# Optimization experiments

Hardware: AMD Instinct MI355X
Metric: run time of the kernel (lower is better)

The kernel has to match this reference:

```python
import jax, jax.numpy as jnp
import numpy as np

NUM_HEADS = 32
NUM_KV = 8
HEAD_DIM = 128


def rotate_half(x):
    half = x.shape[-1] // 2
    x1, x2 = x[..., :half], x[..., half:]
    return jnp.concatenate([-x2, x1], axis=-1)


def apply_rope(x, cos, sin):
    # x: [B, H, S, D]; cos/sin: [S, D] broadcast over batch and heads
    return x * cos + rotate_half(x) * sin


def setup_inputs() -> dict:
    key = jax.random.key(0)
    kx, kqkv, kout = jax.random.split(key, 3)
    B, S, H = 2, 2048, 4096
    x = jax.random.normal(kx, (B, S, H), dtype=jnp.float32)
    Wqkv = jax.random.normal(kqkv, (H, NUM_HEADS * HEAD_DIM + 2 * NUM_KV * HEAD_DIM), dtype=jnp.float32) * (H ** -0.5)
    Wout = jax.random.normal(kout, (H, H), dtype=jnp.float32) * (H ** -0.5)
    # realistic RoPE tables (seq, head_dim)
    inv_freq = 1.0 / (10000.0 ** (np.arange(0, HEAD_DIM, 2, dtype=np.float32) / HEAD_DIM))
    freqs = np.outer(np.arange(S, dtype=np.float32), inv_freq)  # [S, D/2]
    emb = np.concatenate([freqs, freqs], axis=-1)  # [S, D]
    cos = jnp.asarray(np.cos(emb), dtype=jnp.float32)
    sin = jnp.asarray(np.sin(emb), dtype=jnp.float32)
    return {"x": x, "cos": cos, "sin": sin, "Wqkv": Wqkv, "Wout": Wout}


def reference(x, cos, sin, Wqkv, Wout):
    B, S, H = x.shape
    nh, nkv, hd = NUM_HEADS, NUM_KV, HEAD_DIM
    qkv = x @ Wqkv  # [B, S, (nh+2*nkv)*hd]
    q, k, v = jnp.split(qkv, [nh * hd, nh * hd + nkv * hd], axis=-1)
    q = q.reshape(B, S, nh, hd).transpose(0, 2, 1, 3)   # [B, nh, S, hd]
    k = k.reshape(B, S, nkv, hd).transpose(0, 2, 1, 3)  # [B, nkv, S, hd]
    v = v.reshape(B, S, nkv, hd).transpose(0, 2, 1, 3)
    q = apply_rope(q, cos, sin)
    k = apply_rope(k, cos, sin)
    group = nh // nkv
    k = jnp.repeat(k, group, axis=1)  # repeat_interleave over head dim
    v = jnp.repeat(v, group, axis=1)
    scale = 1.0 / jnp.sqrt(jnp.asarray(hd, dtype=x.dtype))
    scores = jnp.einsum('bhqd,bhkd->bhqk', q, k) * scale  # [B, nh, S, S]
    causal = jnp.triu(jnp.ones((S, S), dtype=bool), k=1)
    scores = jnp.where(causal, -jnp.inf, scores)
    w = jax.nn.softmax(scores, axis=-1)
    out = jnp.einsum('bhqk,bhkd->bhqd', w, v)  # [B, nh, S, hd]
    out = out.transpose(0, 2, 1, 3).reshape(B, S, nh * hd)
    return out @ Wout
```

## Files before the change

kernel.cpp:

```cpp
#include <hip/hip_runtime.h>

typedef unsigned short u16;
typedef __attribute__((ext_vector_type(8))) short s16x8;
typedef __attribute__((ext_vector_type(4))) short s16x4;
typedef __attribute__((ext_vector_type(4))) float f32x4;

#define DEVI __device__ __forceinline__

DEVI u16 f2b(float f) {
  union { float f; unsigned u; } v; v.f = f;
  unsigned r = v.u + 0x7FFFu + ((v.u >> 16) & 1u);
  return (u16)(r >> 16);
}
DEVI float b2f(u16 h) {
  union { unsigned u; float f; } v; v.u = ((unsigned)h) << 16;
  return v.f;
}

typedef const __attribute__((address_space(1))) void gas_void;
typedef __attribute__((address_space(3))) void las_void;
DEVI void gload16(const void* g, void* l) {
  __builtin_amdgcn_global_load_lds((gas_void*)g, (las_void*)l, 16, 0, 0);
}

__global__ void conv_bf16(const float* __restrict__ in, u16* __restrict__ out, int n8) {
  int i = blockIdx.x * 256 + threadIdx.x;
  if (i >= n8) return;
  const float* p = in + (size_t)i * 8;
  float4 u = *(const float4*)p;
  float4 v = *(const float4*)(p + 4);
  s16x8 o = {(short)f2b(u.x), (short)f2b(u.y), (short)f2b(u.z), (short)f2b(u.w),
             (short)f2b(v.x), (short)f2b(v.y), (short)f2b(v.z), (short)f2b(v.w)};
  *(s16x8*)(out + (size_t)i * 8) = o;
}

__global__ void trans_bf16(const float* __restrict__ W, u16* __restrict__ Wt, int K, int N) {
  __shared__ __attribute__((aligned(16))) u16 tile[64][68];
  const int t = threadIdx.x;
  const int n0 = blockIdx.x * 64, k0 = blockIdx.y * 64;
#pragma unroll
  for (int i = 0; i < 4; ++i) {
    int c = i * 256 + t;
    int r = c >> 4, q = c & 15;
    float4 v = *(const float4*)(W + (size_t)(k0 + r) * N + n0 + q * 4);
    s16x4 o = {(short)f2b(v.x), (short)f2b(v.y), (short)f2b(v.z), (short)f2b(v.w)};
    *(s16x4*)&tile[r][q * 4] = o;
  }
  __syncthreads();
#pragma unroll
  for (int i = 0; i < 2; ++i) {
    int c = i * 256 + t;
    int n_ = c >> 3, ck = (c & 7) * 8;
    s16x8 o;
#pragma unroll
    for (int j = 0; j < 8; ++j) o[j] = (short)tile[ck + j][n_];
    *(s16x8*)(Wt + (size_t)(n0 + n_) * K + k0 + ck) = o;
  }
}

template <typename TC>
__global__ __launch_bounds__(512, 2) void gemm256(const u16* __restrict__ A,
                                                  const u16* __restrict__ Bt,
                                                  TC* __restrict__ C, int M, int N, int K) {
  __shared__ __attribute__((aligned(16))) u16 As[2][256 * 64];
  __shared__ __attribute__((aligned(16))) u16 Bs[2][256 * 64];
  const int t = threadIdx.x;
  const int nbn = N >> 8;
  const int nwg = (M >> 8) * nbn;
  const int chunk = nwg >> 3;
  const int id = (blockIdx.x & 7) * chunk + (blockIdx.x >> 3);
  const int row0 = (id / nbn) << 8, col0 = (id % nbn) << 8;
  const int w = t >> 6, lane = t & 63, lc = lane & 15, lg = lane >> 4;
  const int wm = (w >> 2) * 128, wn = (w & 3) * 64;
  const int sw7 = lc & 7;

  const f32x4 FZ = {0.f, 0.f, 0.f, 0.f};
  f32x4 acc[8][4];
#pragma unroll
  for (int i = 0; i < 8; ++i)
#pragma unroll
    for (int j = 0; j < 4; ++j) acc[i][j] = FZ;

  const int c_r[4] = {t >> 3, (512 + t) >> 3, (1024 + t) >> 3, (1536 + t) >> 3};
  const int c_s = t & 7;

#define ISSUE_A(i, kt, slot)                                                            \
  gload16(A + (size_t)(row0 + c_r[i]) * K + ((kt) << 6) + ((c_s ^ (c_r[i] & 7)) << 3),  \
          (u16*)As[slot] + ((i) * 512 + t) * 8)
#define ISSUE_B(i, kt, slot)                                                            \
  gload16(Bt + (size_t)(col0 + c_r[i]) * K + ((kt) << 6) + ((c_s ^ (c_r[i] & 7)) << 3), \
          (u16*)Bs[slot] + ((i) * 512 + t) * 8)
#define LOAD_A(MH, AC)                                                            \
  _Pragma("unroll") for (int mf = 0; mf < 4; ++mf)                                \
  _Pragma("unroll") for (int ks = 0; ks < 2; ++ks)                                \
    af[mf][ks] = *(const s16x8*)((AC) + (wm + (MH)*64 + mf * 16 + lc) * 64 +      \
                                 (((ks * 4 + lg) ^ sw7) << 3));
#define LOAD_B(NH, BC)                                                            \
  _Pragma("unroll") for (int nf = 0; nf < 2; ++nf)                                \
  _Pragma("unroll") for (int ks = 0; ks < 2; ++ks)                                \
    bfv[nf][ks] = *(const s16x8*)((BC) + (wn + (NH)*32 + nf * 16 + lc) * 64 +     \
                                  (((ks * 4 + lg) ^ sw7) << 3));
#define MFMA_Q(MH, NH)                                                            \
  _Pragma("unroll") for (int ks = 0; ks < 2; ++ks)                                \
  _Pragma("unroll") for (int mf = 0; mf < 4; ++mf)                                \
  _Pragma("unroll") for (int nf = 0; nf < 2; ++nf)                                \
    acc[(MH)*4 + mf][(NH)*2 + nf] = __builtin_amdgcn_mfma_f32_16x16x32_bf16(      \
        af[mf][ks], bfv[nf][ks], acc[(MH)*4 + mf][(NH)*2 + nf], 0, 0, 0);
#define BAR __builtin_amdgcn_s_barrier()
#define PRIO1 __builtin_amdgcn_s_setprio(1)
#define PRIO0 __builtin_amdgcn_s_setprio(0)

  s16x8 af[4][2], bfv[2][2];
  const int NT = K >> 6;

  ISSUE_A(0, 0, 0); ISSUE_A(1, 0, 0); ISSUE_A(2, 0, 0); ISSUE_A(3, 0, 0);
  ISSUE_B(0, 0, 0); ISSUE_B(1, 0, 0); ISSUE_B(2, 0, 0); ISSUE_B(3, 0, 0);
  asm volatile("s_waitcnt vmcnt(0)" ::: "memory");
  BAR;

  for (int kt = 0; kt < NT; ++kt) {
    const int cur = kt & 1, nxt = cur ^ 1;
    const u16* Ac = As[cur];
    const u16* Bc = Bs[cur];
    LOAD_A(0, Ac)
    LOAD_B(0, Bc)
    if (kt + 1 < NT) {
      ISSUE_A(0, kt + 1, nxt); ISSUE_A(1, kt + 1, nxt);
      ISSUE_A(2, kt + 1, nxt); ISSUE_A(3, kt + 1, nxt);
      ISSUE_B(0, kt + 1, nxt); ISSUE_B(1, kt + 1, nxt);
      ISSUE_B(2, kt + 1, nxt); ISSUE_B(3, kt + 1, nxt);
    }
    BAR; PRIO1; MFMA_Q(0, 0); PRIO0; BAR;
    LOAD_B(1, Bc)
    BAR; PRIO1; MFMA_Q(0, 1); PRIO0; BAR;
    LOAD_A(1, Ac)
    BAR; PRIO1; MFMA_Q(1, 1); PRIO0; BAR;
    LOAD_B(0, Bc)
    BAR; PRIO1; MFMA_Q(1, 0); PRIO0;
    asm volatile("s_waitcnt vmcnt(0)" ::: "memory");
    BAR;
  }
#undef ISSUE_A
#undef ISSUE_B
#undef LOAD_A
#undef LOAD_B
#undef MFMA_Q
#undef BAR
#undef PRIO1
#undef PRIO0

#pragma unroll
  for (int am = 0; am < 8; ++am)
#pragma unroll
    for (int an = 0; an < 4; ++an)
#pragma unroll
      for (int r = 0; r < 4; ++r) {
        const int rg = row0 + wm + (am >> 2) * 64 + (am & 3) * 16 + lg * 4 + r;
        const int cg = col0 + wn + (an >> 1) * 32 + (an & 1) * 16 + lc;
        if constexpr (sizeof(TC) == 2)
          ((u16*)C)[(size_t)rg * N + cg] = f2b(acc[am][an][r]);
        else
          ((float*)C)[(size_t)rg * N + cg] = acc[am][an][r];
      }
}

__global__ void rope_kernel(u16* __restrict__ qkv, const float* __restrict__ cosb,
                            const float* __restrict__ sinb) {
  const int bs = blockIdx.x;
  const int s = bs & 2047;
  u16* row = qkv + (size_t)bs * 6144;
  const float* cr = cosb + s * 128;
  const float* sr = sinb + s * 128;
  for (int p = threadIdx.x; p < 320; p += 256) {
    int head = p >> 3, dc = (p & 7) * 8;
    int ci = head * 128 + dc;
    s16x8 a = *(const s16x8*)&row[ci];
    s16x8 bb = *(const s16x8*)&row[ci + 64];
    float4 c0 = *(const float4*)(cr + dc), c1 = *(const float4*)(cr + dc + 4);
    float4 s0 = *(const float4*)(sr + dc), s1 = *(const float4*)(sr + dc + 4);
    float cv[8] = {c0.x, c0.y, c0.z, c0.w, c1.x, c1.y, c1.z, c1.w};
    float sv[8] = {s0.x, s0.y, s0.z, s0.w, s1.x, s1.y, s1.z, s1.w};
    s16x8 o1, o2;
#pragma unroll
    for (int j = 0; j < 8; ++j) {
      float x1 = b2f((u16)a[j]), x2 = b2f((u16)bb[j]);
      o1[j] = (short)f2b(x1 * cv[j] - x2 * sv[j]);
      o2[j] = (short)f2b(x2 * cv[j] + x1 * sv[j]);
    }
    *(s16x8*)&row[ci] = o1;
    *(s16x8*)&row[ci + 64] = o2;
  }
}

__global__ void vtrans_kernel(const u16* __restrict__ qkv, u16* __restrict__ v_t) {
  __shared__ __attribute__((aligned(16))) u16 tile[64][72];
  const int t = threadIdx.x;
  const int s0 = blockIdx.x * 64;
  const int d0 = blockIdx.y * 64;
  const int bk = blockIdx.z;
  const int b = bk >> 3, kvh = bk & 7;
  const int slot = t & 7, r0 = t >> 3;
#pragma unroll
  for (int i = 0; i < 2; ++i) {
    int s_ = r0 + 32 * i;
    *(s16x8*)&tile[s_][slot * 8] =
        *(const s16x8*)(qkv + (size_t)(b * 2048 + s0 + s_) * 6144 + 5120 + kvh * 128 + d0 + slot * 8);
  }
  __syncthreads();
#pragma unroll
  for (int i = 0; i < 2; ++i) {
    int d_ = r0 + 32 * i;
    s16x8 v;
#pragma unroll
    for (int j = 0; j < 8; ++j) v[j] = (short)tile[slot * 8 + j][d_];
    *(s16x8*)(v_t + ((size_t)bk * 128 + d0 + d_) * 2048 + s0 + slot * 8) = v;
  }
}

__global__ void __launch_bounds__(256, 2) attn_kernel(const u16* __restrict__ qkv,
                                                      const u16* __restrict__ v_t,
                                                      u16* __restrict__ attn) {
  __shared__ __attribute__((aligned(16))) u16 Ks[64][136];
  __shared__ __attribute__((aligned(16))) u16 Vs[128][72];
  __shared__ __attribute__((aligned(16))) u16 Ps[4][32][72];
  const int t = threadIdx.x;
  const int f = blockIdx.x;
  const int xcd = f & 7, ix = f >> 3;
  const int g = (xcd << 1) | (ix >> 6);
  const int r_ = ix & 63;
  const int b = g >> 3, kvh = g & 7;
  const int qt = 15 - (r_ >> 2);
  const int h = kvh * 4 + (r_ & 3);
  const int q0 = qt * 128;
  const int w = t >> 6, lane = t & 63, lc = lane & 15, lg = lane >> 4;
  const int qw = q0 + w * 32;

  const u16* qbase = qkv + (size_t)(b * 2048) * 6144 + h * 128;
  const u16* kbase = qkv + (size_t)(b * 2048) * 6144 + 4096 + kvh * 128;
  const u16* vbase = v_t + (size_t)(b * 8 + kvh) * 128 * 2048;

  s16x8 qf[2][4];
#pragma unroll
  for (int mf = 0; mf < 2; ++mf)
#pragma unroll
    for (int ks = 0; ks < 4; ++ks)
      qf[mf][ks] = *(const s16x8*)(qbase + (size_t)(qw + mf * 16 + lc) * 6144 + ks * 32 + lg * 8);

  const f32x4 FZ = {0.f, 0.f, 0.f, 0.f};
  f32x4 o_acc[2][8];
  float m_run[2][4], l_run[2][4];
#pragma unroll
  for (int mf = 0; mf < 2; ++mf) {
#pragma unroll
    for (int nf = 0; nf < 8; ++nf) o_acc[mf][nf] = FZ;
#pragma unroll
    for (int r = 0; r < 4; ++r) { m_run[mf][r] = -3e38f; l_run[mf][r] = 0.f; }
  }
  const float scale2 = 0.08838834764831845f * 1.44269504088896340736f;

  const int ntiles = q0 / 64 + 2;
  s16x8 kr[4], vr[4];
#pragma unroll
  for (int i = 0; i < 4; ++i) {
    int c = i * 256 + t;
    kr[i] = *(const s16x8*)(kbase + (size_t)(c >> 4) * 6144 + (c & 15) * 8);
    vr[i] = *(const s16x8*)(vbase + (size_t)(c >> 3) * 2048 + (c & 7) * 8);
  }

  for (int kt = 0; kt < ntiles; ++kt) {
    const int k0 = kt * 64;
    __syncthreads();
#pragma unroll
    for (int i = 0; i < 4; ++i) {
      int c = i * 256 + t;
      *(s16x8*)&Ks[c >> 4][(c & 15) * 8] = kr[i];
      *(s16x8*)&Vs[c >> 3][(c & 7) * 8] = vr[i];
    }
    __syncthreads();
    if (kt + 1 < ntiles) {
      int k1 = k0 + 64;
#pragma unroll
      for (int i = 0; i < 4; ++i) {
        int c = i * 256 + t;
        kr[i] = *(const s16x8*)(kbase + (size_t)(k1 + (c >> 4)) * 6144 + (c & 15) * 8);
        vr[i] = *(const s16x8*)(vbase + (size_t)(c >> 3) * 2048 + k1 + (c & 7) * 8);
      }
    }
    if (k0 > qw + 31) continue;

    f32x4 sacc[2][4];
#pragma unroll
    for (int mf = 0; mf < 2; ++mf)
#pragma unroll
      for (int nf = 0; nf < 4; ++nf) sacc[mf][nf] = FZ;
#pragma unroll
    for (int ks = 0; ks < 4; ++ks) {
      s16x8 kf[4];
#pragma unroll
      for (int nf = 0; nf < 4; ++nf)
        kf[nf] = *(const s16x8*)&Ks[nf * 16 + lc][ks * 32 + lg * 8];
#pragma unroll
      for (int mf = 0; mf < 2; ++mf)
#pragma unroll
        for (int nf = 0; nf < 4; ++nf)
          sacc[mf][nf] = __builtin_amdgcn_mfma_f32_16x16x32_bf16(qf[mf][ks], kf[nf], sacc[mf][nf], 0, 0, 0);
    }

#pragma unroll
    for (int mf = 0; mf < 2; ++mf) {
      float pm[4] = {-3e38f, -3e38f, -3e38f, -3e38f};
      const bool dm = (k0 + 63 > qw + mf * 16);
      if (dm) {
#pragma unroll
        for (int nf = 0; nf < 4; ++nf) {
          int kv = k0 + nf * 16 + lc;
#pragma unroll
          for (int r = 0; r < 4; ++r) {
            int qg = qw + mf * 16 + lg * 4 + r;
            float sv = sacc[mf][nf][r] * scale2;
            sv = (kv <= qg) ? sv : -3e38f;
            sacc[mf][nf][r] = sv;
            pm[r] = fmaxf(pm[r], sv);
          }
        }
      } else {
#pragma unroll
        for (int nf = 0; nf < 4; ++nf)
#pragma unroll
          for (int r = 0; r < 4; ++r) {
            float sv = sacc[mf][nf][r] * scale2;
            sacc[mf][nf][r] = sv;
            pm[r] = fmaxf(pm[r], sv);
          }
      }
#pragma unroll
      for (int r = 0; r < 4; ++r) {
        pm[r] = fmaxf(pm[r], __shfl_xor(pm[r], 1));
        pm[r] = fmaxf(pm[r], __shfl_xor(pm[r], 2));
        pm[r] = fmaxf(pm[r], __shfl_xor(pm[r], 4));
        pm[r] = fmaxf(pm[r], __shfl_xor(pm[r], 8));
      }
      bool any = false;
      float mnew[4];
#pragma unroll
      for (int r = 0; r < 4; ++r) {
        mnew[r] = fmaxf(m_run[mf][r], pm[r]);
        any |= (mnew[r] > m_run[mf][r]);
      }
      if (__any(any)) {
#pragma unroll
        for (int r = 0; r < 4; ++r) {
          float fsc = exp2f(m_run[mf][r] - mnew[r]);
          m_run[mf][r] = mnew[r];
          l_run[mf][r] *= fsc;
#pragma unroll
          for (int nf = 0; nf < 8; ++nf) o_acc[mf][nf][r] *= fsc;
        }
      }
      float psum[4] = {0.f, 0.f, 0.f, 0.f};
#pragma unroll
      for (int nf = 0; nf < 4; ++nf)
#pragma unroll
        for (int r = 0; r < 4; ++r) {
          float p = exp2f(sacc[mf][nf][r] - m_run[mf][r]);
          psum[r] += p;
          Ps[w][mf * 16 + lg * 4 + r][nf * 16 + lc] = f2b(p);
        }
#pragma unroll
      for (int r = 0; r < 4; ++r) {
        float ps = psum[r];
        ps += __shfl_xor(ps, 1);
        ps += __shfl_xor(ps, 2);
        ps += __shfl_xor(ps, 4);
        ps += __shfl_xor(ps, 8);
        l_run[mf][r] += ps;
      }
    }
#pragma unroll
    for (int ks = 0; ks < 2; ++ks) {
      s16x8 pf[2];
#pragma unroll
      for (int mf = 0; mf < 2; ++mf)
        pf[mf] = *(const s16x8*)&Ps[w][mf * 16 + lc][ks * 32 + lg * 8];
#pragma unroll
      for (int nf = 0; nf < 8; ++nf) {
        s16x8 vf = *(const s16x8*)&Vs[nf * 16 + lc][ks * 32 + lg * 8];
#pragma unroll
        for (int mf = 0; mf < 2; ++mf)
          o_acc[mf][nf] = __builtin_amdgcn_mfma_f32_16x16x32_bf16(pf[mf], vf, o_acc[mf][nf], 0, 0, 0);
      }
    }
  }

#pragma unroll
  for (int mf = 0; mf < 2; ++mf)
#pragma unroll
    for (int r = 0; r < 4; ++r) {
      float inv = 1.0f / l_run[mf][r];
      int qg = qw + mf * 16 + lg * 4 + r;
#pragma unroll
      for (int nf = 0; nf < 8; ++nf)
        attn[(size_t)(b * 2048 + qg) * 4096 + h * 128 + nf * 16 + lc] =
            f2b(o_acc[mf][nf][r] * inv);
    }
}

extern "C" void kernel_launch(void* const* d_in, const int* in_sizes, int n_in,
                              void* d_out, int out_size, void* d_ws, size_t ws_size,
                              hipStream_t stream) {
  (void)in_sizes; (void)n_in; (void)out_size; (void)ws_size;
  const float* x = (const float*)d_in[0];
  const float* cosb = (const float*)d_in[1];
  const float* sinb = (const float*)d_in[2];
  const float* Wqkv = (const float*)d_in[3];
  const float* Wout = (const float*)d_in[4];
  float* out = (float*)d_out;
  char* ws = (char*)d_ws;

  u16* buf0 = (u16*)ws;
  u16* buf1 = (u16*)(ws + 50331648);
  u16* regc = (u16*)(ws + 100663296);

  conv_bf16<<<8192, 256, 0, stream>>>(x, regc, 2097152);
  trans_bf16<<<dim3(96, 64), 256, 0, stream>>>(Wqkv, buf0, 4096, 6144);
  gemm256<u16><<<384, 512, 0, stream>>>(regc, buf0, buf1, 4096, 6144, 4096);
  rope_kernel<<<4096, 256, 0, stream>>>(buf1, cosb, sinb);
  vtrans_kernel<<<dim3(32, 2, 16), 256, 0, stream>>>(buf1, regc);
  attn_kernel<<<1024, 256, 0, stream>>>(buf1, regc, buf0);
  trans_bf16<<<dim3(64, 64), 256, 0, stream>>>(Wout, regc, 4096, 4096);
  gemm256<float><<<256, 512, 0, stream>>>(buf0, regc, out, 4096, 4096, 4096);
}
```

Before: 627.3 us.

## Split GEMM tiles into half-tiles and stage loads at finer granularity

Restructures the 256x256 bf16 GEMM so that the LDS buffers are split into 128-row half-tiles per operand. Each wave now owns a 64x32 sub-block in each quadrant, where before it held a contiguous 128x64 region. Global-to-LDS loads are issued per half-tile and interleaved between the four MFMA quadrants, with a partial vmcnt(4) wait, so the loop prefetches further ahead and does not drain all loads every k-step. This aims to hide memory latency better, at the cost of more complex scheduling and a loop that assumes NT is even and a power of two for the wraparound indexing.

```diff
diff --git a/kernel.cpp b/kernel.cpp
--- a/kernel.cpp
+++ b/kernel.cpp
@@ -62,8 +62,8 @@
 __global__ __launch_bounds__(512, 2) void gemm256(const u16* __restrict__ A,
                                                   const u16* __restrict__ Bt,
                                                   TC* __restrict__ C, int M, int N, int K) {
-  __shared__ __attribute__((aligned(16))) u16 As[2][256 * 64];
-  __shared__ __attribute__((aligned(16))) u16 Bs[2][256 * 64];
+  __shared__ __attribute__((aligned(16))) u16 As[2][2][128 * 64];
+  __shared__ __attribute__((aligned(16))) u16 Bs[2][2][128 * 64];
   const int t = threadIdx.x;
   const int nbn = N >> 8;
   const int nwg = (M >> 8) * nbn;
@@ -71,97 +71,123 @@
   const int id = (blockIdx.x & 7) * chunk + (blockIdx.x >> 3);
   const int row0 = (id / nbn) << 8, col0 = (id % nbn) << 8;
   const int w = t >> 6, lane = t & 63, lc = lane & 15, lg = lane >> 4;
-  const int wm = (w >> 2) * 128, wn = (w & 3) * 64;
+  const int wqm = (w >> 2) * 64;
+  const int wqn = (w & 3) * 32;
   const int sw7 = lc & 7;
 
   const f32x4 FZ = {0.f, 0.f, 0.f, 0.f};
-  f32x4 acc[8][4];
-#pragma unroll
-  for (int i = 0; i < 8; ++i)
-#pragma unroll
-    for (int j = 0; j < 4; ++j) acc[i][j] = FZ;
-
-  const int c_r[4] = {t >> 3, (512 + t) >> 3, (1024 + t) >> 3, (1536 + t) >> 3};
-  const int c_s = t & 7;
-
-#define ISSUE_A(i, kt, slot)                                                            \
-  gload16(A + (size_t)(row0 + c_r[i]) * K + ((kt) << 6) + ((c_s ^ (c_r[i] & 7)) << 3),  \
-          (u16*)As[slot] + ((i) * 512 + t) * 8)
-#define ISSUE_B(i, kt, slot)                                                            \
-  gload16(Bt + (size_t)(col0 + c_r[i]) * K + ((kt) << 6) + ((c_s ^ (c_r[i] & 7)) << 3), \
-          (u16*)Bs[slot] + ((i) * 512 + t) * 8)
-#define LOAD_A(MH, AC)                                                            \
+  f32x4 acc[4][4][2];
+#pragma unroll
+  for (int q = 0; q < 4; ++q)
+#pragma unroll
+    for (int i = 0; i < 4; ++i)
+#pragma unroll
+      for (int j = 0; j < 2; ++j) acc[q][i][j] = FZ;
+
+  const int s_r0 = t >> 3, s_r1 = (512 + t) >> 3;
+  const int s_s = t & 7;
+
+#define STG_A(kt, H, sl)                                                                   \
+  {                                                                                        \
+    gload16(A + (size_t)(row0 + (H)*128 + s_r0) * K + ((kt) << 6) + ((s_s ^ (s_r0 & 7)) << 3), \
+            (u16*)As[sl][H] + t * 8);                                                      \
+    gload16(A + (size_t)(row0 + (H)*128 + s_r1) * K + ((kt) << 6) + ((s_s ^ (s_r1 & 7)) << 3), \
+            (u16*)As[sl][H] + (512 + t) * 8);                                              \
+  }
+#define STG_B(kt, H, sl)                                                                   \
+  {                                                                                        \
+    gload16(Bt + (size_t)(col0 + (H)*128 + s_r0) * K + ((kt) << 6) + ((s_s ^ (s_r0 & 7)) << 3), \
+            (u16*)Bs[sl][H] + t * 8);                                                      \
+    gload16(Bt + (size_t)(col0 + (H)*128 + s_r1) * K + ((kt) << 6) + ((s_s ^ (s_r1 & 7)) << 3), \
+            (u16*)Bs[sl][H] + (512 + t) * 8);                                              \
+  }
+#define LOAD_A(MH, buf)                                                           \
   _Pragma("unroll") for (int mf = 0; mf < 4; ++mf)                                \
   _Pragma("unroll") for (int ks = 0; ks < 2; ++ks)                                \
-    af[mf][ks] = *(const s16x8*)((AC) + (wm + (MH)*64 + mf * 16 + lc) * 64 +      \
+    af[mf][ks] = *(const s16x8*)(As[buf][MH] + (wqm + mf * 16 + lc) * 64 +        \
                                  (((ks * 4 + lg) ^ sw7) << 3));
-#define LOAD_B(NH, BC)                                                            \
+#define LOAD_B(NH, buf, DST)                                                      \
   _Pragma("unroll") for (int nf = 0; nf < 2; ++nf)                                \
   _Pragma("unroll") for (int ks = 0; ks < 2; ++ks)                                \
-    bfv[nf][ks] = *(const s16x8*)((BC) + (wn + (NH)*32 + nf * 16 + lc) * 64 +     \
+    DST[nf][ks] = *(const s16x8*)(Bs[buf][NH] + (wqn + nf * 16 + lc) * 64 +       \
                                   (((ks * 4 + lg) ^ sw7) << 3));
-#define MFMA_Q(MH, NH)                                                            \
+#define MFMA_Q(q, BV)                                                             \
   _Pragma("unroll") for (int ks = 0; ks < 2; ++ks)                                \
   _Pragma("unroll") for (int mf = 0; mf < 4; ++mf)                                \
   _Pragma("unroll") for (int nf = 0; nf < 2; ++nf)                                \
-    acc[(MH)*4 + mf][(NH)*2 + nf] = __builtin_amdgcn_mfma_f32_16x16x32_bf16(      \
-        af[mf][ks], bfv[nf][ks], acc[(MH)*4 + mf][(NH)*2 + nf], 0, 0, 0);
+    acc[q][mf][nf] = __builtin_amdgcn_mfma_f32_16x16x32_bf16(                     \
+        af[mf][ks], BV[nf][ks], acc[q][mf][nf], 0, 0, 0);
 #define BAR __builtin_amdgcn_s_barrier()
 #define PRIO1 __builtin_amdgcn_s_setprio(1)
 #define PRIO0 __builtin_amdgcn_s_setprio(0)
-
-  s16x8 af[4][2], bfv[2][2];
-  const int NT = K >> 6;
-
-  ISSUE_A(0, 0, 0); ISSUE_A(1, 0, 0); ISSUE_A(2, 0, 0); ISSUE_A(3, 0, 0);
-  ISSUE_B(0, 0, 0); ISSUE_B(1, 0, 0); ISSUE_B(2, 0, 0); ISSUE_B(3, 0, 0);
+#define WAIT4 asm volatile("s_waitcnt vmcnt(4)" ::: "memory")
+
+  s16x8 af[4][2], bfv0[2][2], bfv1[2][2];
+  const int NT = K >> 6, NI = NT >> 1, TM = NT - 1;
+
+  STG_A(0, 0, 0) STG_B(0, 0, 0) STG_B(0, 1, 0) STG_A(0, 1, 0)
+  STG_A(1, 0, 1) STG_B(1, 1, 1)
+  WAIT4;
+  BAR;
+
+  for (int i = 0; i < NI; ++i) {
+    const int t1 = 2 * i + 1;
+    const int t2 = (2 * i + 2) & TM, t3 = (2 * i + 3) & TM;
+    LOAD_A(0, 0) LOAD_B(0, 0, bfv0)
+    STG_B(t1, 0, 1)
+    BAR; PRIO1; MFMA_Q(0, bfv0) PRIO0; BAR;
+    LOAD_B(1, 0, bfv1)
+    STG_A(t1, 1, 1)
+    BAR; PRIO1; MFMA_Q(1, bfv1) PRIO0; BAR;
+    LOAD_A(1, 0)
+    STG_A(t2, 0, 0)
+    BAR; PRIO1; MFMA_Q(2, bfv1) PRIO0; BAR;
+    STG_B(t2, 1, 0)
+    BAR; PRIO1; MFMA_Q(3, bfv0) PRIO0;
+    WAIT4;
+    BAR;
+    LOAD_A(0, 1) LOAD_B(0, 1, bfv0)
+    STG_B(t2, 0, 0)
+    BAR; PRIO1; MFMA_Q(0, bfv0) PRIO0; BAR;
+    LOAD_B(1, 1, bfv1)
+    STG_A(t2, 1, 0)
+    BAR; PRIO1; MFMA_Q(1, bfv1) PRIO0; BAR;
+    LOAD_A(1, 1)
+    STG_A(t3, 0, 1)
+    BAR; PRIO1; MFMA_Q(2, bfv1) PRIO0; BAR;
+    STG_B(t3, 1, 1)
+    BAR; PRIO1; MFMA_Q(3, bfv0) PRIO0;
+    WAIT4;
+    BAR;
+  }
   asm volatile("s_waitcnt vmcnt(0)" ::: "memory");
   BAR;
-
-  for (int kt = 0; kt < NT; ++kt) {
-    const int cur = kt & 1, nxt = cur ^ 1;
-    const u16* Ac = As[cur];
-    const u16* Bc = Bs[cur];
-    LOAD_A(0, Ac)
-    LOAD_B(0, Bc)
-    if (kt + 1 < NT) {
-      ISSUE_A(0, kt + 1, nxt); ISSUE_A(1, kt + 1, nxt);
-      ISSUE_A(2, kt + 1, nxt); ISSUE_A(3, kt + 1, nxt);
-      ISSUE_B(0, kt + 1, nxt); ISSUE_B(1, kt + 1, nxt);
-      ISSUE_B(2, kt + 1, nxt); ISSUE_B(3, kt + 1, nxt);
-    }
-    BAR; PRIO1; MFMA_Q(0, 0); PRIO0; BAR;
-    LOAD_B(1, Bc)
-    BAR; PRIO1; MFMA_Q(0, 1); PRIO0; BAR;
-    LOAD_A(1, Ac)
-    BAR; PRIO1; MFMA_Q(1, 1); PRIO0; BAR;
-    LOAD_B(0, Bc)
-    BAR; PRIO1; MFMA_Q(1, 0); PRIO0;
-    asm volatile("s_waitcnt vmcnt(0)" ::: "memory");
-    BAR;
-  }
-#undef ISSUE_A
-#undef ISSUE_B
+#undef STG_A
+#undef STG_B
 #undef LOAD_A
 #undef LOAD_B
 #undef MFMA_Q
 #undef BAR
 #undef PRIO1
 #undef PRIO0
-
-#pragma unroll
-  for (int am = 0; am < 8; ++am)
-#pragma unroll
-    for (int an = 0; an < 4; ++an)
-#pragma unroll
-      for (int r = 0; r < 4; ++r) {
-        const int rg = row0 + wm + (am >> 2) * 64 + (am & 3) * 16 + lg * 4 + r;
-        const int cg = col0 + wn + (an >> 1) * 32 + (an & 1) * 16 + lc;
-        if constexpr (sizeof(TC) == 2)
-          ((u16*)C)[(size_t)rg * N + cg] = f2b(acc[am][an][r]);
-        else
-          ((float*)C)[(size_t)rg * N + cg] = acc[am][an][r];
-      }
+#undef WAIT4
+
+  const int qmh[4] = {0, 0, 1, 1}, qnh[4] = {0, 1, 1, 0};
+#pragma unroll
+  for (int q = 0; q < 4; ++q)
+#pragma unroll
+    for (int mf = 0; mf < 4; ++mf)
+#pragma unroll
+      for (int nf = 0; nf < 2; ++nf)
+#pragma unroll
+        for (int r = 0; r < 4; ++r) {
+          const int rg = row0 + qmh[q] * 128 + wqm + mf * 16 + lg * 4 + r;
+          const int cg = col0 + qnh[q] * 128 + wqn + nf * 16 + lc;
+          if constexpr (sizeof(TC) == 2)
+            ((u16*)C)[(size_t)rg * N + cg] = f2b(acc[q][mf][nf][r]);
+          else
+            ((float*)C)[(size_t)rg * N + cg] = acc[q][mf][nf][r];
+        }
 }
 
 __global__ void rope_kernel(u16* __restrict__ qkv, const float* __restrict__ cosb,
```

New measurement: 580.1 us. -7.5%, faster.
